# Optimization experiments

Hardware: AMD Instinct MI355X
Metric: run time of the kernel (lower is better)

The kernel has to match this reference:

```python
import jax, jax.numpy as jnp
import numpy as np

B, T, H, NSPK = 8, 1024, 1024, 2
LN_EPS = 1e-5


def setup_inputs() -> dict:
    key = jax.random.key(0)
    ks = jax.random.split(key, 12)
    s = 1.0 / np.sqrt(H)
    return {
        "x": jax.random.normal(ks[0], (B, T, H), jnp.float32),
        "qmask": jax.random.uniform(ks[1], (B, T, NSPK), jnp.float32),
        "dia_len": jax.random.randint(ks[2], (B,), T // 2, T + 1),
        "wp": 8,
        "wf": 8,
        "W_msg": jax.random.normal(ks[3], (H, H), jnp.float32) * s,
        "b_msg": jax.random.normal(ks[4], (H,), jnp.float32) * s,
        "W_self": jax.random.normal(ks[5], (H, H), jnp.float32) * s,
        "b_self": jax.random.normal(ks[6], (H,), jnp.float32) * s,
        "W_out": jax.random.normal(ks[7], (H, H), jnp.float32) * s,
        "b_out": jax.random.normal(ks[8], (H,), jnp.float32) * s,
        "gamma": jnp.ones((H,), jnp.float32),
        "beta": jnp.zeros((H,), jnp.float32),
    }


def reference(x, qmask, dia_len, wp, wf, W_msg, b_msg, W_self, b_self, W_out, b_out, gamma, beta):
    Bb, Tt, Hh = x.shape
    spk = jnp.argmax(qmask, axis=-1)                     # [B,T]
    pos = jnp.arange(Tt)
    offs = jnp.arange(-wp, wf + 1)                       # [W]
    idx = pos[:, None] + offs[None, :]                   # [T,W] window indices
    vlen = dia_len[:, None, None]                        # [B,1,1]
    valid = (idx[None] >= 0) & (idx[None] <= vlen - 1)   # [B,T,W]
    idxc = jnp.clip(idx, 0, Tt - 1)
    nb = jnp.take(x, idxc, axis=1)                       # [B,T,W,H]
    nb_spk = jnp.take(spk, idxc, axis=1)                 # [B,T,W]
    same = (nb_spk == spk[:, :, None]).astype(x.dtype)
    w = jnp.where(valid, 0.5 + 0.5 * same, 0.0)          # speaker weights, masked
    cnt = jnp.maximum(valid.sum(-1).astype(x.dtype), 1.0)  # window sizes [B,T]
    msg = jnp.einsum('btw,btwh->bth', w, nb) / cnt[..., None]
    h = x @ W_self + b_self + msg @ W_msg + b_msg        # per-node fusion
    node_valid = (pos[None, :] < dia_len[:, None])[..., None]
    out = jnp.where(node_valid, h, x)                    # nodes past dia_len keep x
    y = jax.nn.relu(out) @ W_out + b_out                 # dropout = identity (eval)
    z = x + y
    mean = z.mean(-1, keepdims=True)
    var = z.var(-1, keepdims=True)
    return gamma * (z - mean) / jnp.sqrt(var + LN_EPS) + beta
```

## Files before the change

### kernel.cpp

```cpp
#include <hip/hip_runtime.h>


typedef unsigned short u16;
typedef float floatx4 __attribute__((ext_vector_type(4)));
typedef short shortx8 __attribute__((ext_vector_type(8)));

#define T_ 1024
#define H_ 1024

__device__ __forceinline__ float bf2f(u16 v) {
    return __uint_as_float(((unsigned)v) << 16);
}
__device__ __forceinline__ u16 f2bf(float f) {
    unsigned u = __float_as_uint(f);
    return (u16)((u + 0x7fffu + ((u >> 16) & 1u)) >> 16);
}
__device__ __forceinline__ void async16(const void* g, void* l) {
    __builtin_amdgcn_global_load_lds(
        (__attribute__((address_space(1))) void*)g,
        (__attribute__((address_space(3))) void*)l, 16, 0, 0);
}

__global__ __launch_bounds__(256)
void transpose_pack(const float* __restrict__ Wself, const float* __restrict__ Wmsg,
                    const float* __restrict__ Wout,
                    u16* __restrict__ wt_cat, u16* __restrict__ wt_out)
{
    __shared__ float s[32][33];
    const int wid = blockIdx.z;
    const float* src = (wid == 0) ? Wself : ((wid == 1) ? Wmsg : Wout);
    const int n0 = blockIdx.x * 32, k0 = blockIdx.y * 32;
    const int tx = threadIdx.x & 31, ty = threadIdx.x >> 5;
#pragma unroll
    for (int i = 0; i < 4; ++i) {
        int k = k0 + ty + 8 * i;
        s[ty + 8 * i][tx] = src[(size_t)k * H_ + n0 + tx];
    }
    __syncthreads();
#pragma unroll
    for (int i = 0; i < 4; ++i) {
        int n = n0 + ty + 8 * i;
        u16 v = f2bf(s[tx][ty + 8 * i]);
        if (wid < 2) wt_cat[(size_t)n * 2048 + wid * 1024 + k0 + tx] = v;
        else         wt_out[(size_t)n * 1024 + k0 + tx] = v;
    }
}

__global__ __launch_bounds__(256)
void msg_pack(const float* __restrict__ x, const float* __restrict__ qmask,
              const int* __restrict__ dia_len, u16* __restrict__ xcat)
{
    __shared__ u16 sx[32][1024];
    const int tid = threadIdx.x;
    const int b = blockIdx.y;
    const int t0 = blockIdx.x * 16;
    const int dlen = dia_len[b];
    const int c4 = tid * 4;
    const float* xb = x + (size_t)b * T_ * H_;

    unsigned spkmask = 0;
#pragma unroll 4
    for (int r = 0; r < 32; ++r) {
        int row = t0 - 8 + r;
        row = row < 0 ? 0 : (row > T_ - 1 ? T_ - 1 : row);
        const float* q = qmask + ((size_t)b * T_ + row) * 2;
        spkmask |= (q[1] > q[0] ? 1u : 0u) << r;
        float4 v = *(const float4*)(xb + (size_t)row * H_ + c4);
        ushort4 u;
        u.x = f2bf(v.x); u.y = f2bf(v.y); u.z = f2bf(v.z); u.w = f2bf(v.w);
        *(ushort4*)&sx[r][c4] = u;
    }
    __syncthreads();

    for (int lt = 0; lt < 16; ++lt) {
        const int t = t0 + lt;
        const unsigned cs = (spkmask >> (lt + 8)) & 1u;
        float a0 = 0.f, a1 = 0.f, a2 = 0.f, a3 = 0.f;
        int cnt = 0;
#pragma unroll
        for (int o = 0; o < 17; ++o) {
            const int idx = t + o - 8;
            if (idx >= 0 && idx < dlen) {
                const float w = (((spkmask >> (lt + o)) & 1u) == cs) ? 1.0f : 0.5f;
                ++cnt;
                ushort4 u = *(const ushort4*)&sx[lt + o][c4];
                a0 += w * bf2f(u.x); a1 += w * bf2f(u.y);
                a2 += w * bf2f(u.z); a3 += w * bf2f(u.w);
            }
        }
        const float inv = 1.0f / (float)(cnt > 0 ? cnt : 1);
        ushort4 m;
        m.x = f2bf(a0 * inv); m.y = f2bf(a1 * inv);
        m.z = f2bf(a2 * inv); m.w = f2bf(a3 * inv);
        const size_t rowg = (size_t)b * T_ + t;
        *(ushort4*)&xcat[rowg * 2048 + 1024 + c4] = m;
        *(ushort4*)&xcat[rowg * 2048 + c4] = *(const ushort4*)&sx[lt + 8][c4];
    }
}

template <int K, int EPI>
__global__ __launch_bounds__(256)
void gemm_bt(const u16* __restrict__ A, const u16* __restrict__ Bt,
             const float* __restrict__ bias1, const float* __restrict__ bias2,
             const float* __restrict__ X, const int* __restrict__ dia_len,
             u16* __restrict__ Rout, float* __restrict__ Zout)
{
    __shared__ u16 sA[128 * 32];
    __shared__ u16 sB[128 * 32];
    const int tid = threadIdx.x;
    const int bn = blockIdx.x * 128;
    const int bm = blockIdx.y * 128;
    const int wave = tid >> 6, lane = tid & 63;
    const int wr = wave >> 1, wc = wave & 1;
    const int lrow = lane & 15, lq = lane >> 4;

    const u16* gA0 = A + (size_t)(bm + (tid >> 2)) * K + (tid & 3) * 8;
    const u16* gA1 = gA0 + (size_t)64 * K;
    const u16* gB0 = Bt + (size_t)(bn + (tid >> 2)) * K + (tid & 3) * 8;
    const u16* gB1 = gB0 + (size_t)64 * K;
    u16* lA = sA + wave * 512;
    u16* lB = sB + wave * 512;

    floatx4 acc[4][4];
#pragma unroll
    for (int i = 0; i < 4; ++i)
#pragma unroll
        for (int j = 0; j < 4; ++j)
            acc[i][j] = (floatx4){0.f, 0.f, 0.f, 0.f};

    const u16* pa = sA + (wr * 64 + lrow) * 32 + lq * 8;
    const u16* pb = sB + (wc * 64 + lrow) * 32 + lq * 8;

    for (int k0 = 0; k0 < K; k0 += 32) {
        __syncthreads();
        async16(gA0 + k0, lA);
        async16(gA1 + k0, lA + 2048);
        async16(gB0 + k0, lB);
        async16(gB1 + k0, lB + 2048);
        __syncthreads();
        shortx8 av[4], bv[4];
#pragma unroll
        for (int i = 0; i < 4; ++i) av[i] = *(const shortx8*)(pa + i * 512);
#pragma unroll
        for (int j = 0; j < 4; ++j) bv[j] = *(const shortx8*)(pb + j * 512);
#pragma unroll
        for (int i = 0; i < 4; ++i)
#pragma unroll
            for (int j = 0; j < 4; ++j)
                acc[i][j] = __builtin_amdgcn_mfma_f32_16x16x32_bf16(
                    av[i], bv[j], acc[i][j], 0, 0, 0);
    }

    const int dl = (EPI == 1) ? dia_len[bm >> 10] : 0;
#pragma unroll
    for (int i = 0; i < 4; ++i) {
        const int row0 = bm + wr * 64 + i * 16 + lq * 4;
#pragma unroll
        for (int j = 0; j < 4; ++j) {
            const int col = bn + wc * 64 + j * 16 + lrow;
#pragma unroll
            for (int r = 0; r < 4; ++r) {
                const int row = row0 + r;
                const float v = acc[i][j][r];
                if (EPI == 1) {
                    const float h = v + bias1[col] + bias2[col];
                    const float xv = X[(size_t)row * H_ + col];
                    const float outv = ((row & (T_ - 1)) < dl) ? h : xv;
                    Rout[(size_t)row * H_ + col] = f2bf(fmaxf(outv, 0.f));
                } else {
                    const float z = X[(size_t)row * H_ + col] + v + bias1[col];
                    Zout[(size_t)row * H_ + col] = z;
                }
            }
        }
    }
}

__global__ __launch_bounds__(256)
void ln_kernel(const float* __restrict__ Z, const float* __restrict__ gamma,
               const float* __restrict__ beta, float* __restrict__ out)
{
    const int row = blockIdx.x;
    const int tid = threadIdx.x;
    const size_t base = (size_t)row * H_ + tid * 4;
    float4 v = *(const float4*)(Z + base);
    float s = v.x + v.y + v.z + v.w;
    float q = v.x * v.x + v.y * v.y + v.z * v.z + v.w * v.w;
#pragma unroll
    for (int off = 32; off > 0; off >>= 1) {
        s += __shfl_down(s, off);
        q += __shfl_down(q, off);
    }
    __shared__ float ps[4], pq[4];
    const int wave = tid >> 6, lane = tid & 63;
    if (lane == 0) { ps[wave] = s; pq[wave] = q; }
    __syncthreads();
    const float S = ps[0] + ps[1] + ps[2] + ps[3];
    const float Q = pq[0] + pq[1] + pq[2] + pq[3];
    const float mean = S * (1.0f / 1024.0f);
    const float var = Q * (1.0f / 1024.0f) - mean * mean;
    const float inv = rsqrtf(var + 1e-5f);
    float4 g = *(const float4*)(gamma + tid * 4);
    float4 bt = *(const float4*)(beta + tid * 4);
    float4 o;
    o.x = g.x * (v.x - mean) * inv + bt.x;
    o.y = g.y * (v.y - mean) * inv + bt.y;
    o.z = g.z * (v.z - mean) * inv + bt.z;
    o.w = g.w * (v.w - mean) * inv + bt.w;
    *(float4*)(out + base) = o;
}

extern "C" void kernel_launch(void* const* d_in, const int* in_sizes, int n_in,
                              void* d_out, int out_size, void* d_ws, size_t ws_size,
                              hipStream_t stream)
{
    (void)in_sizes; (void)n_in; (void)out_size; (void)ws_size;
    const float* x       = (const float*)d_in[0];
    const float* qmask   = (const float*)d_in[1];
    const int*   dia_len = (const int*)d_in[2];
    const float* W_msg   = (const float*)d_in[5];
    const float* b_msg   = (const float*)d_in[6];
    const float* W_self  = (const float*)d_in[7];
    const float* b_self  = (const float*)d_in[8];
    const float* W_out   = (const float*)d_in[9];
    const float* b_out   = (const float*)d_in[10];
    const float* gamma   = (const float*)d_in[11];
    const float* beta    = (const float*)d_in[12];
    float* out = (float*)d_out;

    char* ws = (char*)d_ws;
    u16*   xcat   = (u16*)ws;
    u16*   rbuf   = (u16*)(ws + (size_t)(32u << 20));
    u16*   wt_cat = (u16*)(ws + (size_t)(48u << 20));
    u16*   wt_out = (u16*)(ws + (size_t)(52u << 20));
    float* zbuf   = (float*)ws;

    transpose_pack<<<dim3(32, 32, 3), 256, 0, stream>>>(W_self, W_msg, W_out, wt_cat, wt_out);
    msg_pack<<<dim3(64, 8), 256, 0, stream>>>(x, qmask, dia_len, xcat);
    gemm_bt<2048, 1><<<dim3(8, 64), 256, 0, stream>>>(xcat, wt_cat, b_self, b_msg,
                                                      x, dia_len, rbuf, nullptr);
    gemm_bt<1024, 2><<<dim3(8, 64), 256, 0, stream>>>(rbuf, wt_out, b_out, nullptr,
                                                      x, nullptr, nullptr, zbuf);
    ln_kernel<<<dim3(8192), 256, 0, stream>>>(zbuf, gamma, beta, out);
}
```

Baseline: 230.8 us.

## Multi-buffer GEMM LDS loads with a four-stage async pipeline

Replaces the single LDS tile buffer in the bf16 MFMA GEMM with four rotating buffers. Three k-tiles are prefetched through async global-to-LDS loads, with explicit vmcnt waits and one barrier per iteration, so loads for future tiles overlap current MFMA work and one of the two barriers per k-step goes away. The epilogue also reads X only for rows past dia_len. The cost is four times the LDS per block, which may lower occupancy.

```diff
diff --git a/kernel.cpp b/kernel.cpp
--- a/kernel.cpp
+++ b/kernel.cpp
@@ -105,8 +105,9 @@
              const float* __restrict__ X, const int* __restrict__ dia_len,
              u16* __restrict__ Rout, float* __restrict__ Zout)
 {
-    __shared__ u16 sA[128 * 32];
-    __shared__ u16 sB[128 * 32];
+    constexpr int NT = K / 32;
+    __shared__ u16 sA[4][128 * 32];
+    __shared__ u16 sB[4][128 * 32];
     const int tid = threadIdx.x;
     const int bn = blockIdx.x * 128;
     const int bm = blockIdx.y * 128;
@@ -118,31 +119,48 @@
     const u16* gA1 = gA0 + (size_t)64 * K;
     const u16* gB0 = Bt + (size_t)(bn + (tid >> 2)) * K + (tid & 3) * 8;
     const u16* gB1 = gB0 + (size_t)64 * K;
-    u16* lA = sA + wave * 512;
-    u16* lB = sB + wave * 512;
-
-    floatx4 acc[4][4];
-#pragma unroll
-    for (int i = 0; i < 4; ++i)
-#pragma unroll
-        for (int j = 0; j < 4; ++j)
-            acc[i][j] = (floatx4){0.f, 0.f, 0.f, 0.f};
-
-    const u16* pa = sA + (wr * 64 + lrow) * 32 + lq * 8;
-    const u16* pb = sB + (wc * 64 + lrow) * 32 + lq * 8;
-
-    for (int k0 = 0; k0 < K; k0 += 32) {
-        __syncthreads();
+    const int lofs = wave * 512;
+
+    auto stage = [&](int t) {
+        const int s = t & 3;
+        const int k0 = t * 32;
+        u16* lA = &sA[s][0] + lofs;
+        u16* lB = &sB[s][0] + lofs;
         async16(gA0 + k0, lA);
         async16(gA1 + k0, lA + 2048);
         async16(gB0 + k0, lB);
         async16(gB1 + k0, lB + 2048);
-        __syncthreads();
+    };
+
+    floatx4 acc[4][4];
+#pragma unroll
+    for (int i = 0; i < 4; ++i)
+#pragma unroll
+        for (int j = 0; j < 4; ++j)
+            acc[i][j] = (floatx4){0.f, 0.f, 0.f, 0.f};
+
+    const int pao = (wr * 64 + lrow) * 32 + lq * 8;
+    const int pbo = (wc * 64 + lrow) * 32 + lq * 8;
+
+    stage(0); stage(1); stage(2);
+
+    for (int t = 0; t < NT; ++t) {
+        if (t < NT - 2)       asm volatile("s_waitcnt vmcnt(8)" ::: "memory");
+        else if (t == NT - 2) asm volatile("s_waitcnt vmcnt(4)" ::: "memory");
+        else                  asm volatile("s_waitcnt vmcnt(0)" ::: "memory");
+        __builtin_amdgcn_s_barrier();
+        asm volatile("" ::: "memory");
+
+        const u16* pa = &sA[t & 3][0] + pao;
+        const u16* pb = &sB[t & 3][0] + pbo;
         shortx8 av[4], bv[4];
 #pragma unroll
         for (int i = 0; i < 4; ++i) av[i] = *(const shortx8*)(pa + i * 512);
 #pragma unroll
         for (int j = 0; j < 4; ++j) bv[j] = *(const shortx8*)(pb + j * 512);
+
+        if (t + 3 < NT) stage(t + 3);
+
 #pragma unroll
         for (int i = 0; i < 4; ++i)
 #pragma unroll
@@ -164,8 +182,12 @@
                 const float v = acc[i][j][r];
                 if (EPI == 1) {
                     const float h = v + bias1[col] + bias2[col];
-                    const float xv = X[(size_t)row * H_ + col];
-                    const float outv = ((row & (T_ - 1)) < dl) ? h : xv;
+                    float outv;
+                    if ((row & (T_ - 1)) < dl) {
+                        outv = h;
+                    } else {
+                        outv = X[(size_t)row * H_ + col];
+                    }
                     Rout[(size_t)row * H_ + col] = f2bf(fmaxf(outv, 0.f));
                 } else {
                     const float z = X[(size_t)row * H_ + col] + v + bias1[col];
```

Result: no change. 235.4 us (+2.0%).
